# Kernel optimization log

Measured on AMD Instinct MI355X. Metric: run time of the kernel, lower is better.

## Reference

```python
import jax, jax.numpy as jnp
import numpy as np

B = 512        # events (graphs) in batch
NPE = 512      # nodes per event (structured so knn can be batched)
N = B * NPE    # total nodes = 262144
K = 6          # knn neighbors
F_IN = 128     # 2 * n_samples
H = 16         # conv1 out
OUT = 10       # graph_out
COORD_MAX = 16 # detector grid extent


def setup_inputs() -> dict:
    key = jax.random.key(0)
    k1, k2, k3, k4 = jax.random.split(key, 4)
    xy = jax.random.randint(k1, (N, 2), 0, COORD_MAX, dtype=jnp.int32)
    batch = jnp.repeat(jnp.arange(B, dtype=jnp.int32), NPE)  # coo[:,2] = event id
    coo = jnp.concatenate([xy, batch[:, None]], axis=1)       # [N,3] int
    x = jax.random.normal(k2, (N, F_IN), dtype=jnp.float32)
    W1 = jax.random.normal(k3, (F_IN, H), dtype=jnp.float32) * (1.0 / np.sqrt(F_IN))
    b1 = jnp.zeros((H,), dtype=jnp.float32)
    W2 = jax.random.normal(k4, (H, OUT), dtype=jnp.float32) * (1.0 / np.sqrt(H))
    b2 = jnp.zeros((OUT,), dtype=jnp.float32)
    return {"coo": coo, "x": x, "W1": W1, "b1": b1, "W2": W2, "b2": b2}


def knn_edges(coo):
    # knn_graph(coo, K, batch=coo[:,2], loop=False): batches are contiguous
    # blocks of NPE nodes, so reshape and do per-event brute-force knn.
    pos = coo.astype(jnp.float32).reshape(B, NPE, 3)
    # squared pairwise distances per event: [B, n, n]
    d = jnp.sum((pos[:, :, None, :] - pos[:, None, :, :]) ** 2, axis=-1)
    d = d + jnp.eye(NPE, dtype=d.dtype) * 1e9  # exclude self (loop=False)
    _, idx = jax.lax.top_k(-d, K)              # [B, n, K] neighbor indices (local)
    base = (jnp.arange(B, dtype=jnp.int32) * NPE)[:, None, None]
    src = (idx.astype(jnp.int32) + base).reshape(-1)                       # j (neighbor)
    dst = jnp.broadcast_to(jnp.arange(NPE, dtype=jnp.int32)[None, :, None] + base,
                           (B, NPE, K)).reshape(-1)                        # i (center)
    return src, dst


def gcn_conv(x, W, b, src, dst):
    # GCNConv: out = D^{-1/2} (A + I) D^{-1/2} X W + b
    loops = jnp.arange(N, dtype=jnp.int32)
    row = jnp.concatenate([dst, loops])  # target
    col = jnp.concatenate([src, loops])  # source
    deg = jax.ops.segment_sum(jnp.ones_like(row, dtype=x.dtype), row, num_segments=N)
    dinv = jnp.where(deg > 0, jax.lax.rsqrt(deg), 0.0)
    norm = dinv[row] * dinv[col]         # [E]
    h = x @ W                            # [N, F_out]
    msg = h[col] * norm[:, None]         # gather + scale
    return jax.ops.segment_sum(msg, row, num_segments=N) + b


def reference(coo, x, W1, b1, W2, b2):
    src, dst = knn_edges(coo)
    h = jax.nn.relu(gcn_conv(x, W1, b1, src, dst))
    out = gcn_conv(h, W2, b2, src, dst)  # [N, OUT] per-node output (n_lin == 0)
    return out
```

## Files before the change

### kernel.cpp

```cpp
#include <hip/hip_runtime.h>
#include <hip/hip_bf16.h>

#define NPE   512
#define F_IN  128
#define HDIM  16
#define ODIM  10

typedef __attribute__((ext_vector_type(8))) short short8;
typedef __attribute__((ext_vector_type(4))) float f32x4;

static __device__ __forceinline__ unsigned pkbf(float lo, float hi) {
  __hip_bfloat162 h = __float22bfloat162_rn(make_float2(lo, hi));
  unsigned r;
  __builtin_memcpy(&r, &h, 4);
  return r;
}
static __device__ __forceinline__ short f2bf(float f) {
  __hip_bfloat16 h = __float2bfloat16(f);
  short r;
  __builtin_memcpy(&r, &h, 2);
  return r;
}
static __device__ __forceinline__ float bflo(unsigned d) {
  return __builtin_bit_cast(float, d << 16);
}
static __device__ __forceinline__ float bfhi(unsigned d) {
  return __builtin_bit_cast(float, d & 0xffff0000u);
}
static __device__ __forceinline__ unsigned umin2(unsigned a, unsigned b) { return a < b ? a : b; }
static __device__ __forceinline__ unsigned umax2(unsigned a, unsigned b) { return a > b ? a : b; }

__global__ __launch_bounds__(512, 4) void gnet_fused(
    const int* __restrict__ coo, const float* __restrict__ x,
    const float* __restrict__ W1, const float* __restrict__ b1,
    const float* __restrict__ W2, const float* __restrict__ b2,
    float* __restrict__ out)
{
  __shared__ __align__(16) short    hbuf[NPE][24];
  __shared__ __align__(16) short    r_s [NPE][24];
  __shared__ unsigned short cellof_s[NPE];
  __shared__ unsigned       cnt_s [256];
  __shared__ unsigned       scan_s[256];
  __shared__ unsigned       cur_s [256];
  __shared__ unsigned short bucket_s[NPE];
  __shared__ unsigned       top7_s[256][8];
  __shared__ unsigned       tile_c;
  __shared__ unsigned       sortflag;

  const int tid   = threadIdx.x;
  const int gbase = blockIdx.x * NPE;
  const int ln    = tid & 63;
  const int wv    = tid >> 6;
  const int lcol  = ln & 15;
  const int lkg   = ln >> 4;

  const int cx = coo[(gbase + tid) * 3 + 0];
  const int cy = coo[(gbase + tid) * 3 + 1];
  const int mycell = cy * 16 + cx;
  cellof_s[tid] = (unsigned short)mycell;
  if (tid == 0) { tile_c = 0; sortflag = 0; }
  __syncthreads();

  short8 bw1[4];
#pragma unroll
  for (int s = 0; s < 4; ++s) {
#pragma unroll
    for (int e = 0; e < 8; ++e) {
      const int k = s * 32 + lkg * 8 + e;
      bw1[s][e] = f2bf(W1[k * HDIM + lcol]);
    }
  }

  if (wv == 0) {
#pragma unroll
    for (int q = 0; q < 4; ++q) cnt_s[ln * 4 + q] = 0;
    __threadfence_block();
#pragma unroll
    for (int q = 0; q < 8; ++q)
      atomicAdd(&cnt_s[cellof_s[ln + q * 64]], 1u);
    __threadfence_block();
    const unsigned c0 = cnt_s[ln * 4 + 0], c1 = cnt_s[ln * 4 + 1];
    const unsigned c2 = cnt_s[ln * 4 + 2], c3 = cnt_s[ln * 4 + 3];
    const unsigned psum = c0 + c1 + c2 + c3;
    unsigned sv = psum;
#pragma unroll
    for (int off = 1; off < 64; off <<= 1) {
      unsigned u = __shfl_up(sv, off, 64);
      if (ln >= off) sv += u;
    }
    const unsigned basex = sv - psum;
    const unsigned e0 = basex + c0, e1 = e0 + c1, e2 = e1 + c2, e3 = e2 + c3;
    scan_s[ln * 4 + 0] = e0; cur_s[ln * 4 + 0] = e0 - c0;
    scan_s[ln * 4 + 1] = e1; cur_s[ln * 4 + 1] = e1 - c1;
    scan_s[ln * 4 + 2] = e2; cur_s[ln * 4 + 2] = e2 - c2;
    scan_s[ln * 4 + 3] = e3; cur_s[ln * 4 + 3] = e3 - c3;
    __threadfence_block();
#pragma unroll
    for (int q = 0; q < 8; ++q) {
      const int node = ln + q * 64;
      const unsigned slot = atomicAdd(&cur_s[cellof_s[node]], 1u);
      bucket_s[slot] = (unsigned short)node;
    }
    __threadfence_block();
    if (ln == 0) *(volatile unsigned*)&sortflag = 1u;
  } else if (wv < 4) {
    while (*(volatile unsigned*)&sortflag == 0u) __builtin_amdgcn_s_sleep(8);
    __threadfence_block();
  }

  if (wv < 4 && cnt_s[tid] != 0) {
    const int ccx = tid & 15, ccy = tid >> 4;
    unsigned k0 = 0x7fffffffu, k1 = k0, k2 = k0, k3 = k0, k4 = k0, k5 = k0, k6 = k0;
    auto insert7 = [&](unsigned key) {
      if (key < k6) {
        k6 = key;
        unsigned lo, hi;
        lo = umin2(k5, k6); hi = umax2(k5, k6); k5 = lo; k6 = hi;
        lo = umin2(k4, k5); hi = umax2(k4, k5); k4 = lo; k5 = hi;
        lo = umin2(k3, k4); hi = umax2(k3, k4); k3 = lo; k4 = hi;
        lo = umin2(k2, k3); hi = umax2(k2, k3); k2 = lo; k3 = hi;
        lo = umin2(k1, k2); hi = umax2(k1, k2); k1 = lo; k2 = hi;
        lo = umin2(k0, k1); hi = umax2(k0, k1); k0 = lo; k1 = hi;
      }
    };
    auto scan_cell = [&](int c, unsigned kb) {
      const unsigned e = scan_s[c];
      const unsigned n = cnt_s[c];
      for (unsigned q = e - n; q < e; ++q) insert7(kb | (unsigned)bucket_s[q]);
    };
    scan_cell(tid, 0u);
    for (int r = 1; r <= 15; ++r) {
      const unsigned r2 = (unsigned)(r * r);
      if (r2 > (k6 >> 9)) break;
      for (int sg = 0; sg < 2; ++sg) {
        const int yy = ccy + (sg ? r : -r);
        if (yy < 0 || yy > 15) continue;
        const int xlo = ccx - r < 0 ? 0 : ccx - r;
        const int xhi = ccx + r > 15 ? 15 : ccx + r;
        for (int xx = xlo; xx <= xhi; ++xx) {
          const int dx = xx - ccx;
          const unsigned kb = (unsigned)(dx * dx + (int)r2) << 9;
          if (kb < k6) scan_cell(yy * 16 + xx, kb);
        }
      }
      for (int sg = 0; sg < 2; ++sg) {
        const int xx = ccx + (sg ? r : -r);
        if (xx < 0 || xx > 15) continue;
        const int ylo = ccy - r + 1 < 0 ? 0 : ccy - r + 1;
        const int yhi = ccy + r - 1 > 15 ? 15 : ccy + r - 1;
        for (int yy = ylo; yy <= yhi; ++yy) {
          const int dy = yy - ccy;
          const unsigned kb = (unsigned)(dy * dy + (int)r2) << 9;
          if (kb < k6) scan_cell(yy * 16 + xx, kb);
        }
      }
    }
    unsigned* tp = top7_s[tid];
    tp[0] = k0; tp[1] = k1; tp[2] = k2; tp[3] = k3; tp[4] = k4; tp[5] = k5; tp[6] = k6;
  }

  for (;;) {
    int t = 0;
    if (ln == 0) t = (int)atomicAdd(&tile_c, 1u);
    t = __shfl(t, 0, 64);
    if (t >= 16) break;
    const int base = t * 32;
    const float4* pA = reinterpret_cast<const float4*>(
        x + (size_t)(gbase + base + lcol) * F_IN + lkg * 8);
    const float4* pB = reinterpret_cast<const float4*>(
        x + (size_t)(gbase + base + 16 + lcol) * F_IN + lkg * 8);
    float4 a0 = pA[0],  a1 = pA[1],  a2 = pA[8],  a3 = pA[9];
    float4 a4 = pA[16], a5 = pA[17], a6 = pA[24], a7 = pA[25];
    float4 b0 = pB[0],  b1v = pB[1], b2v = pB[8], b3 = pB[9];
    float4 b4 = pB[16], b5 = pB[17], b6 = pB[24], b7 = pB[25];

    f32x4 accA = {0.f, 0.f, 0.f, 0.f};
    f32x4 accB = {0.f, 0.f, 0.f, 0.f};
    const float4 av[8] = {a0, a1, a2, a3, a4, a5, a6, a7};
    const float4 bv[8] = {b0, b1v, b2v, b3, b4, b5, b6, b7};
#pragma unroll
    for (int s = 0; s < 4; ++s) {
      const float4 u = av[2 * s], v = av[2 * s + 1];
      uint4 pk = {pkbf(u.x, u.y), pkbf(u.z, u.w), pkbf(v.x, v.y), pkbf(v.z, v.w)};
      short8 af = __builtin_bit_cast(short8, pk);
      accA = __builtin_amdgcn_mfma_f32_16x16x32_bf16(af, bw1[s], accA, 0, 0, 0);
    }
#pragma unroll
    for (int s = 0; s < 4; ++s) {
      const float4 u = bv[2 * s], v = bv[2 * s + 1];
      uint4 pk = {pkbf(u.x, u.y), pkbf(u.z, u.w), pkbf(v.x, v.y), pkbf(v.z, v.w)};
      short8 bf = __builtin_bit_cast(short8, pk);
      accB = __builtin_amdgcn_mfma_f32_16x16x32_bf16(bf, bw1[s], accB, 0, 0, 0);
    }
#pragma unroll
    for (int i = 0; i < 4; ++i) {
      hbuf[base + lkg * 4 + i][lcol]      = f2bf(accA[i]);
      hbuf[base + 16 + lkg * 4 + i][lcol] = f2bf(accB[i]);
    }
  }
  __syncthreads();

  const unsigned* tp = top7_s[mycell];
  const unsigned t0 = tp[0], t1 = tp[1], t2 = tp[2], t3 = tp[3];
  const unsigned t4 = tp[4], t5 = tp[5], t6 = tp[6];
  const unsigned selfkey = (unsigned)tid;
  int p = 7;
  p = (t6 == selfkey) ? 6 : p;
  p = (t5 == selfkey) ? 5 : p;
  p = (t4 == selfkey) ? 4 : p;
  p = (t3 == selfkey) ? 3 : p;
  p = (t2 == selfkey) ? 2 : p;
  p = (t1 == selfkey) ? 1 : p;
  p = (t0 == selfkey) ? 0 : p;
  const int nb0 = (int)((p > 0 ? t0 : t1) & 511u);
  const int nb1 = (int)((p > 1 ? t1 : t2) & 511u);
  const int nb2 = (int)((p > 2 ? t2 : t3) & 511u);
  const int nb3 = (int)((p > 3 ? t3 : t4) & 511u);
  const int nb4 = (int)((p > 4 ? t4 : t5) & 511u);
  const int nb5 = (int)((p > 5 ? t5 : t6) & 511u);

  {
    float acc[HDIM];
#pragma unroll
    for (int o = 0; o < HDIM; ++o) acc[o] = 0.f;
    const int rows[7] = {tid, nb0, nb1, nb2, nb3, nb4, nb5};
#pragma unroll
    for (int r = 0; r < 7; ++r) {
      const unsigned* hp = reinterpret_cast<const unsigned*>(hbuf[rows[r]]);
      const uint4 ha = *reinterpret_cast<const uint4*>(hp);
      const uint4 hb = *reinterpret_cast<const uint4*>(hp + 4);
      const unsigned hd[8] = {ha.x, ha.y, ha.z, ha.w, hb.x, hb.y, hb.z, hb.w};
#pragma unroll
      for (int q = 0; q < 8; ++q) {
        acc[2 * q]     += bflo(hd[q]);
        acc[2 * q + 1] += bfhi(hd[q]);
      }
    }
    const float inv = 1.0f / 7.0f;
    unsigned* rp = reinterpret_cast<unsigned*>(r_s[tid]);
#pragma unroll
    for (int q = 0; q < 8; ++q) {
      const float v0 = fmaxf(acc[2 * q]     * inv + b1[2 * q],     0.f);
      const float v1 = fmaxf(acc[2 * q + 1] * inv + b1[2 * q + 1], 0.f);
      rp[q] = pkbf(v0, v1);
    }
  }
  __syncthreads();

  float* h2f = reinterpret_cast<float*>(hbuf);
  short8 bw2 = {0, 0, 0, 0, 0, 0, 0, 0};
  if (lkg < 2 && lcol < ODIM) {
#pragma unroll
    for (int e = 0; e < 8; ++e) {
      const int k = lkg * 8 + e;
      bw2[e] = f2bf(W2[k * ODIM + lcol]);
    }
  }
#pragma unroll
  for (int t = 0; t < 4; ++t) {
    const int nt = wv * 64 + t * 16;
    short8 af = {0, 0, 0, 0, 0, 0, 0, 0};
    if (lkg < 2) {
      af = *reinterpret_cast<const short8*>(&r_s[nt + lcol][lkg * 8]);
    }
    f32x4 acc = {0.f, 0.f, 0.f, 0.f};
    acc = __builtin_amdgcn_mfma_f32_16x16x32_bf16(af, bw2, acc, 0, 0, 0);
#pragma unroll
    for (int i = 0; i < 4; ++i) {
      if (lcol < ODIM) h2f[(nt + lkg * 4 + i) * 12 + lcol] = acc[i];
    }
  }
  __syncthreads();

  {
    f32x4 s0 = {0.f, 0.f, 0.f, 0.f}, s1 = s0, s2 = s0;
    const int rows[7] = {tid, nb0, nb1, nb2, nb3, nb4, nb5};
#pragma unroll
    for (int r = 0; r < 7; ++r) {
      const f32x4* hp = reinterpret_cast<const f32x4*>(h2f + rows[r] * 12);
      s0 += hp[0]; s1 += hp[1]; s2 += hp[2];
    }
    const float inv = 1.0f / 7.0f;
    float acc[12];
#pragma unroll
    for (int c = 0; c < 4; ++c) { acc[c] = s0[c]; acc[4 + c] = s1[c]; acc[8 + c] = s2[c]; }
    float* op = out + (size_t)(gbase + tid) * ODIM;
#pragma unroll
    for (int c = 0; c < ODIM; c += 2) {
      float2 v;
      v.x = acc[c]     * inv + b2[c];
      v.y = acc[c + 1] * inv + b2[c + 1];
      *reinterpret_cast<float2*>(op + c) = v;
    }
  }
}

extern "C" void kernel_launch(void* const* d_in, const int* in_sizes, int n_in,
                              void* d_out, int out_size, void* d_ws, size_t ws_size,
                              hipStream_t stream) {
  const int*   coo = (const int*)  d_in[0];
  const float* x   = (const float*)d_in[1];
  const float* W1  = (const float*)d_in[2];
  const float* b1  = (const float*)d_in[3];
  const float* W2  = (const float*)d_in[4];
  const float* b2  = (const float*)d_in[5];
  gnet_fused<<<dim3(512), dim3(512), 0, stream>>>(coo, x, W1, b1, W2, b2,
                                                  (float*)d_out);
}
```

Before: 34.13 us.

## Double-buffer x loads in layer-1 GEMM and aggregate before W2 matmul

The layer-1 projection loop now uses 16-row tiles with a double-buffered load pipeline: the next tile's x loads are issued before the current tile is computed, to hide global memory latency. Layer 2 is reordered so the neighbor aggregation happens on the 16-wide hidden features first, with the W2 MFMA applied afterwards. Its results go straight to global memory instead of through an LDS float buffer and a second gather pass. This reorder adds an extra bf16 rounding of the aggregated hidden features. r_s padding is also removed (row stride 24 to 16), which may raise LDS bank conflicts.

Measured after the change: 37.09 us. +8.7%, slower.

```diff
diff --git a/kernel.cpp b/kernel.cpp
--- a/kernel.cpp
+++ b/kernel.cpp
@@ -37,7 +37,7 @@
     float* __restrict__ out)
 {
   __shared__ __align__(16) short    hbuf[NPE][24];
-  __shared__ __align__(16) short    r_s [NPE][24];
+  __shared__ __align__(16) short    r_s [NPE][16];
   __shared__ unsigned short cellof_s[NPE];
   __shared__ unsigned       cnt_s [256];
   __shared__ unsigned       scan_s[256];
@@ -159,43 +159,51 @@
     tp[0] = k0; tp[1] = k1; tp[2] = k2; tp[3] = k3; tp[4] = k4; tp[5] = k5; tp[6] = k6;
   }
 
-  for (;;) {
-    int t = 0;
-    if (ln == 0) t = (int)atomicAdd(&tile_c, 1u);
-    t = __shfl(t, 0, 64);
-    if (t >= 16) break;
-    const int base = t * 32;
-    const float4* pA = reinterpret_cast<const float4*>(
-        x + (size_t)(gbase + base + lcol) * F_IN + lkg * 8);
-    const float4* pB = reinterpret_cast<const float4*>(
-        x + (size_t)(gbase + base + 16 + lcol) * F_IN + lkg * 8);
-    float4 a0 = pA[0],  a1 = pA[1],  a2 = pA[8],  a3 = pA[9];
-    float4 a4 = pA[16], a5 = pA[17], a6 = pA[24], a7 = pA[25];
-    float4 b0 = pB[0],  b1v = pB[1], b2v = pB[8], b3 = pB[9];
-    float4 b4 = pB[16], b5 = pB[17], b6 = pB[24], b7 = pB[25];
-
-    f32x4 accA = {0.f, 0.f, 0.f, 0.f};
-    f32x4 accB = {0.f, 0.f, 0.f, 0.f};
-    const float4 av[8] = {a0, a1, a2, a3, a4, a5, a6, a7};
-    const float4 bv[8] = {b0, b1v, b2v, b3, b4, b5, b6, b7};
-#pragma unroll
-    for (int s = 0; s < 4; ++s) {
-      const float4 u = av[2 * s], v = av[2 * s + 1];
-      uint4 pk = {pkbf(u.x, u.y), pkbf(u.z, u.w), pkbf(v.x, v.y), pkbf(v.z, v.w)};
-      short8 af = __builtin_bit_cast(short8, pk);
-      accA = __builtin_amdgcn_mfma_f32_16x16x32_bf16(af, bw1[s], accA, 0, 0, 0);
-    }
-#pragma unroll
-    for (int s = 0; s < 4; ++s) {
-      const float4 u = bv[2 * s], v = bv[2 * s + 1];
-      uint4 pk = {pkbf(u.x, u.y), pkbf(u.z, u.w), pkbf(v.x, v.y), pkbf(v.z, v.w)};
-      short8 bf = __builtin_bit_cast(short8, pk);
-      accB = __builtin_amdgcn_mfma_f32_16x16x32_bf16(bf, bw1[s], accB, 0, 0, 0);
-    }
-#pragma unroll
-    for (int i = 0; i < 4; ++i) {
-      hbuf[base + lkg * 4 + i][lcol]      = f2bf(accA[i]);
-      hbuf[base + 16 + lkg * 4 + i][lcol] = f2bf(accB[i]);
+  {
+    auto steal = [&]() -> unsigned {
+      unsigned t = 0;
+      if (ln == 0) t = atomicAdd(&tile_c, 1u);
+      return (unsigned)__shfl((int)t, 0, 64);
+    };
+    auto issue8 = [&](float4* buf, unsigned t) {
+      const unsigned rb = umin2(t, 31u) * 16u;
+      const float4* q = reinterpret_cast<const float4*>(
+          x + (size_t)(gbase + rb + lcol) * F_IN + lkg * 8);
+      buf[0] = q[0];  buf[1] = q[1];  buf[2] = q[8];  buf[3] = q[9];
+      buf[4] = q[16]; buf[5] = q[17]; buf[6] = q[24]; buf[7] = q[25];
+    };
+    auto compute16 = [&](const float4* buf, unsigned t) {
+      const unsigned rb = umin2(t, 31u) * 16u;
+      f32x4 acc = {0.f, 0.f, 0.f, 0.f};
+#pragma unroll
+      for (int s = 0; s < 4; ++s) {
+        const float4 u = buf[2 * s], v = buf[2 * s + 1];
+        uint4 pk = {pkbf(u.x, u.y), pkbf(u.z, u.w), pkbf(v.x, v.y), pkbf(v.z, v.w)};
+        short8 af = __builtin_bit_cast(short8, pk);
+        acc = __builtin_amdgcn_mfma_f32_16x16x32_bf16(af, bw1[s], acc, 0, 0, 0);
+      }
+#pragma unroll
+      for (int i = 0; i < 4; ++i) {
+        hbuf[rb + lkg * 4 + i][lcol] = f2bf(acc[i]);
+      }
+    };
+
+    float4 bufA[8], bufB[8];
+    unsigned tCur = steal();
+    issue8(bufA, tCur);
+    for (;;) {
+      unsigned tNext = steal();
+      issue8(bufB, tNext);
+      compute16(bufA, tCur);
+      bool done = tCur >= 32u;
+      tCur = tNext;
+      if (done) break;
+      tNext = steal();
+      issue8(bufA, tNext);
+      compute16(bufB, tCur);
+      done = tCur >= 32u;
+      tCur = tNext;
+      if (done) break;
     }
   }
   __syncthreads();
@@ -218,17 +226,17 @@
   const int nb3 = (int)((p > 3 ? t3 : t4) & 511u);
   const int nb4 = (int)((p > 4 ? t4 : t5) & 511u);
   const int nb5 = (int)((p > 5 ? t5 : t6) & 511u);
+  const int rows[7] = {tid, nb0, nb1, nb2, nb3, nb4, nb5};
 
   {
     float acc[HDIM];
 #pragma unroll
     for (int o = 0; o < HDIM; ++o) acc[o] = 0.f;
-    const int rows[7] = {tid, nb0, nb1, nb2, nb3, nb4, nb5};
 #pragma unroll
     for (int r = 0; r < 7; ++r) {
-      const unsigned* hp = reinterpret_cast<const unsigned*>(hbuf[rows[r]]);
-      const uint4 ha = *reinterpret_cast<const uint4*>(hp);
-      const uint4 hb = *reinterpret_cast<const uint4*>(hp + 4);
+      const uint4* hp = reinterpret_cast<const uint4*>(&hbuf[rows[r]][0]);
+      const uint4 ha = hp[0];
+      const uint4 hb = hp[1];
       const unsigned hd[8] = {ha.x, ha.y, ha.z, ha.w, hb.x, hb.y, hb.z, hb.w};
 #pragma unroll
       for (int q = 0; q < 8; ++q) {
@@ -237,60 +245,72 @@
       }
     }
     const float inv = 1.0f / 7.0f;
-    unsigned* rp = reinterpret_cast<unsigned*>(r_s[tid]);
+    unsigned pk[8];
 #pragma unroll
     for (int q = 0; q < 8; ++q) {
       const float v0 = fmaxf(acc[2 * q]     * inv + b1[2 * q],     0.f);
       const float v1 = fmaxf(acc[2 * q + 1] * inv + b1[2 * q + 1], 0.f);
-      rp[q] = pkbf(v0, v1);
-    }
+      pk[q] = pkbf(v0, v1);
+    }
+    uint4* rp = reinterpret_cast<uint4*>(&r_s[tid][0]);
+    rp[0] = make_uint4(pk[0], pk[1], pk[2], pk[3]);
+    rp[1] = make_uint4(pk[4], pk[5], pk[6], pk[7]);
   }
   __syncthreads();
 
-  float* h2f = reinterpret_cast<float*>(hbuf);
-  short8 bw2 = {0, 0, 0, 0, 0, 0, 0, 0};
-  if (lkg < 2 && lcol < ODIM) {
-#pragma unroll
-    for (int e = 0; e < 8; ++e) {
-      const int k = lkg * 8 + e;
-      bw2[e] = f2bf(W2[k * ODIM + lcol]);
-    }
-  }
-#pragma unroll
-  for (int t = 0; t < 4; ++t) {
-    const int nt = wv * 64 + t * 16;
-    short8 af = {0, 0, 0, 0, 0, 0, 0, 0};
-    if (lkg < 2) {
-      af = *reinterpret_cast<const short8*>(&r_s[nt + lcol][lkg * 8]);
-    }
-    f32x4 acc = {0.f, 0.f, 0.f, 0.f};
-    acc = __builtin_amdgcn_mfma_f32_16x16x32_bf16(af, bw2, acc, 0, 0, 0);
-#pragma unroll
-    for (int i = 0; i < 4; ++i) {
-      if (lcol < ODIM) h2f[(nt + lkg * 4 + i) * 12 + lcol] = acc[i];
-    }
+  {
+    float acc[HDIM];
+#pragma unroll
+    for (int o = 0; o < HDIM; ++o) acc[o] = 0.f;
+#pragma unroll
+    for (int r = 0; r < 7; ++r) {
+      const uint4* hp = reinterpret_cast<const uint4*>(&r_s[rows[r]][0]);
+      const uint4 ha = hp[0];
+      const uint4 hb = hp[1];
+      const unsigned hd[8] = {ha.x, ha.y, ha.z, ha.w, hb.x, hb.y, hb.z, hb.w};
+#pragma unroll
+      for (int q = 0; q < 8; ++q) {
+        acc[2 * q]     += bflo(hd[q]);
+        acc[2 * q + 1] += bfhi(hd[q]);
+      }
+    }
+    const float inv = 1.0f / 7.0f;
+    unsigned pk[8];
+#pragma unroll
+    for (int q = 0; q < 8; ++q) {
+      pk[q] = pkbf(acc[2 * q] * inv, acc[2 * q + 1] * inv);
+    }
+    uint4* ap = reinterpret_cast<uint4*>(&hbuf[tid][0]);
+    ap[0] = make_uint4(pk[0], pk[1], pk[2], pk[3]);
+    ap[1] = make_uint4(pk[4], pk[5], pk[6], pk[7]);
   }
   __syncthreads();
 
   {
-    f32x4 s0 = {0.f, 0.f, 0.f, 0.f}, s1 = s0, s2 = s0;
-    const int rows[7] = {tid, nb0, nb1, nb2, nb3, nb4, nb5};
-#pragma unroll
-    for (int r = 0; r < 7; ++r) {
-      const f32x4* hp = reinterpret_cast<const f32x4*>(h2f + rows[r] * 12);
-      s0 += hp[0]; s1 += hp[1]; s2 += hp[2];
-    }
-    const float inv = 1.0f / 7.0f;
-    float acc[12];
-#pragma unroll
-    for (int c = 0; c < 4; ++c) { acc[c] = s0[c]; acc[4 + c] = s1[c]; acc[8 + c] = s2[c]; }
-    float* op = out + (size_t)(gbase + tid) * ODIM;
-#pragma unroll
-    for (int c = 0; c < ODIM; c += 2) {
-      float2 v;
-      v.x = acc[c]     * inv + b2[c];
-      v.y = acc[c + 1] * inv + b2[c + 1];
-      *reinterpret_cast<float2*>(op + c) = v;
+    short8 bw2 = {0, 0, 0, 0, 0, 0, 0, 0};
+    if (lkg < 2 && lcol < ODIM) {
+#pragma unroll
+      for (int e = 0; e < 8; ++e) {
+        const int k = lkg * 8 + e;
+        bw2[e] = f2bf(W2[k * ODIM + lcol]);
+      }
+    }
+    const float b2v = (lcol < ODIM) ? b2[lcol] : 0.f;
+#pragma unroll
+    for (int t = 0; t < 4; ++t) {
+      const int nt = wv * 64 + t * 16;
+      short8 af = {0, 0, 0, 0, 0, 0, 0, 0};
+      if (lkg < 2) {
+        af = *reinterpret_cast<const short8*>(&hbuf[nt + lcol][lkg * 8]);
+      }
+      f32x4 acc = {0.f, 0.f, 0.f, 0.f};
+      acc = __builtin_amdgcn_mfma_f32_16x16x32_bf16(af, bw2, acc, 0, 0, 0);
+      if (lcol < ODIM) {
+#pragma unroll
+        for (int i = 0; i < 4; ++i) {
+          out[(size_t)(gbase + nt + lkg * 4 + i) * ODIM + lcol] = acc[i] + b2v;
+        }
+      }
     }
   }
 }
```
